# Kernel tuning notes

Hardware: AMD Instinct MI355X
Metric: run time of the kernel (lower is better)

## Reference

```python
import jax, jax.numpy as jnp
import numpy as np
import math

N_HEADS = 16
ROPE_BASE = 10000.0


def _rope_interleaved(t, cos, sin):
    # t: [B,H,T,dk]; cos/sin: [T, dk//2] broadcast over B,H
    te, to = t[..., 0::2], t[..., 1::2]
    re = te * cos - to * sin
    ro = te * sin + to * cos
    # interleave back: [..., dk//2, 2] -> [..., dk]
    return jnp.stack([re, ro], axis=-1).reshape(t.shape)


def setup_inputs() -> dict:
    key = jax.random.key(0)
    ks = jax.random.split(key, 5)
    B, T, C = 2, 2048, 1024
    s = 1.0 / math.sqrt(C)
    return {
        "x": jax.random.normal(ks[0], (B, T, C), dtype=jnp.float32),
        "W_qkv": jax.random.normal(ks[1], (C, 3 * C), dtype=jnp.float32) * s,
        "b_qkv": jax.random.normal(ks[2], (3 * C,), dtype=jnp.float32) * 0.02,
        "W_proj": jax.random.normal(ks[3], (C, C), dtype=jnp.float32) * s,
        "b_proj": jax.random.normal(ks[4], (C,), dtype=jnp.float32) * 0.02,
    }


def reference(x, W_qkv, b_qkv, W_proj, b_proj):
    B, T, C = x.shape
    H = N_HEADS
    dk = C // H

    qkv = x @ W_qkv + b_qkv                      # [B,T,3C]
    q, k, v = jnp.split(qkv, 3, axis=-1)
    q = q.reshape(B, T, H, dk).transpose(0, 2, 1, 3)  # [B,H,T,dk]
    k = k.reshape(B, T, H, dk).transpose(0, 2, 1, 3)
    v = v.reshape(B, T, H, dk).transpose(0, 2, 1, 3)

    # RoPE angles: pos * base^(-2i/dk)
    freqs = ROPE_BASE ** (-2.0 * jnp.arange(dk // 2, dtype=jnp.float32) / dk)
    angles = jnp.arange(T, dtype=jnp.float32)[:, None] * freqs[None, :]  # [T,dk//2]
    cos, sin = jnp.cos(angles), jnp.sin(angles)

    q = _rope_interleaved(q, cos, sin)
    k = _rope_interleaved(k, cos, sin)

    attn = jnp.einsum("bhqd,bhkd->bhqk", q, k) / math.sqrt(dk)  # [B,H,T,T]
    causal = jnp.triu(jnp.full((T, T), -jnp.inf, dtype=attn.dtype), k=1)
    attn = jax.nn.softmax(attn + causal, axis=-1)

    scores = jnp.einsum("bhqk,bhkd->bhqd", attn, v)  # [B,H,T,dk]
    scores = scores.transpose(0, 2, 1, 3).reshape(B, T, C)
    return scores @ W_proj + b_proj
```

## Files before the change

### kernel.cpp

```cpp
#include <hip/hip_runtime.h>
#include <hip/hip_bf16.h>

typedef __bf16 bf16x8 __attribute__((ext_vector_type(8)));
typedef float f32x4 __attribute__((ext_vector_type(4)));
typedef float f32x16 __attribute__((ext_vector_type(16)));
typedef unsigned short u16;
typedef u16 u16x8 __attribute__((ext_vector_type(8)));

__device__ __forceinline__ u16 f2bf(float f) {
  union { float f; unsigned u; } v; v.f = f;
  unsigned r = v.u + 0x7fffu + ((v.u >> 16) & 1u);
  return (u16)(r >> 16);
}
__device__ __forceinline__ float bf2f(u16 u) {
  union { unsigned u; float f; } v; v.u = (unsigned)u << 16; return v.f;
}
__device__ __forceinline__ unsigned cvtpk(float a, float b) {
  unsigned r;
  asm("v_cvt_pk_bf16_f32 %0, %1, %2" : "=v"(r) : "v"(a), "v"(b));
  return r;
}
__device__ __forceinline__ float exp2_(float x) {
  float r;
  asm("v_exp_f32 %0, %1" : "=v"(r) : "v"(x));
  return r;
}
__device__ __forceinline__ void gload16(const void* g, void* l) {
  __builtin_amdgcn_global_load_lds(
      (__attribute__((address_space(1))) void*)(void*)g,
      (__attribute__((address_space(3))) void*)l, 16, 0, 0);
}

union U8 { bf16x8 v; unsigned u[4]; };

__global__ __launch_bounds__(256) void cast_x_k(const float* __restrict__ x,
                                                u16* __restrict__ xb, int n8) {
  int id = blockIdx.x * 256 + threadIdx.x;
  if (id >= n8) return;
  const float4* p = (const float4*)(x + (size_t)id * 8);
  float4 a = p[0], b = p[1];
  u16x8 o;
  o[0] = f2bf(a.x); o[1] = f2bf(a.y); o[2] = f2bf(a.z); o[3] = f2bf(a.w);
  o[4] = f2bf(b.x); o[5] = f2bf(b.y); o[6] = f2bf(b.z); o[7] = f2bf(b.w);
  *(u16x8*)(xb + (size_t)id * 8) = o;
}

__global__ __launch_bounds__(256) void tcast_k(const float* __restrict__ W,
                                               u16* __restrict__ Wt, int R, int Cc) {
  __shared__ float tile[32][33];
  int bx = blockIdx.x * 32, by = blockIdx.y * 32;
  int tx = threadIdx.x & 31, ty = threadIdx.x >> 5;
#pragma unroll
  for (int j = 0; j < 4; j++)
    tile[ty + j * 8][tx] = W[(size_t)(by + ty + j * 8) * Cc + bx + tx];
  __syncthreads();
#pragma unroll
  for (int j = 0; j < 4; j++)
    Wt[(size_t)(bx + ty + j * 8) * R + by + tx] = f2bf(tile[tx][ty + j * 8]);
}

template <bool BF16OUT>
__global__ __launch_bounds__(256) void gemm_bt_k(const u16* __restrict__ A,
                                                 const u16* __restrict__ Bt,
                                                 const float* __restrict__ bias,
                                                 void* __restrict__ Cv,
                                                 int M, int N, int K) {
  __shared__ u16 As[128 * 64];
  __shared__ u16 Bs[128 * 64];
  int tid = threadIdx.x;
  int m0 = blockIdx.y * 128, n0 = blockIdx.x * 128;
  int wave = tid >> 6, lane = tid & 63;
  int wm = (wave & 1) * 64, wn = (wave >> 1) * 64;
  int lrow = lane & 15, lk = (lane >> 4) * 8;
  int rr = lane >> 3, cb = (lane & 7) * 16;

  f32x4 acc[4][4] = {};

  for (int k0 = 0; k0 < K; k0 += 64) {
#pragma unroll
    for (int i = 0; i < 4; i++) {
      int row = wave * 32 + i * 8 + rr;
      int cc = (cb ^ ((row & 7) << 4)) >> 1;
      gload16(A + (size_t)(m0 + row) * K + k0 + cc, &As[(wave * 32 + i * 8) * 64]);
      gload16(Bt + (size_t)(n0 + row) * K + k0 + cc, &Bs[(wave * 32 + i * 8) * 64]);
    }
    __syncthreads();
#pragma unroll
    for (int kk = 0; kk < 2; kk++) {
      bf16x8 af[4], bfr[4];
#pragma unroll
      for (int i = 0; i < 4; i++) {
        int arow = wm + i * 16 + lrow;
        int ab = (arow * 128 + (kk * 32 + lk) * 2) ^ ((arow & 7) << 4);
        af[i] = *(const bf16x8*)((const char*)As + ab);
        int brow = wn + i * 16 + lrow;
        int bb = (brow * 128 + (kk * 32 + lk) * 2) ^ ((brow & 7) << 4);
        bfr[i] = *(const bf16x8*)((const char*)Bs + bb);
      }
#pragma unroll
      for (int i = 0; i < 4; i++)
#pragma unroll
        for (int j = 0; j < 4; j++)
          acc[i][j] = __builtin_amdgcn_mfma_f32_16x16x32_bf16(af[i], bfr[j], acc[i][j], 0, 0, 0);
    }
    __syncthreads();
  }
  int rg = lane >> 4;
#pragma unroll
  for (int i = 0; i < 4; i++) {
#pragma unroll
    for (int j = 0; j < 4; j++) {
      int col = n0 + wn + j * 16 + lrow;
      float bz = bias ? bias[col] : 0.f;
#pragma unroll
      for (int r = 0; r < 4; r++) {
        int row = m0 + wm + i * 16 + rg * 4 + r;
        float val = acc[i][j][r] + bz;
        if constexpr (BF16OUT)
          ((u16*)Cv)[(size_t)row * N + col] = f2bf(val);
        else
          ((float*)Cv)[(size_t)row * N + col] = val;
      }
    }
  }
}

__global__ __launch_bounds__(256) void rope_qk_k(const u16* __restrict__ qkv,
                                                 u16* __restrict__ qb,
                                                 u16* __restrict__ kfb) {
  int id = blockIdx.x * 256 + threadIdx.x;
  int i = id & 31;
  int h = (id >> 5) & 15;
  int t = (id >> 9) & 2047;
  int b = id >> 20;
  size_t row = (size_t)b * 2048 + t;
  const u16* base = qkv + row * 3072 + h * 64 + 2 * i;
  ushort2 qp = *(const ushort2*)(base);
  ushort2 kp = *(const ushort2*)(base + 1024);
  float qx = bf2f(qp.x), qy = bf2f(qp.y), kx = bf2f(kp.x), ky = bf2f(kp.y);
  float freq = exp2f((float)i * -0.41524101186092029f);
  float ang = (float)t * freq;
  float sv, cv;
  sincosf(ang, &sv, &cv);
  const float QS = 0.18033688011112042f;
  int bh = b * 16 + h;
  size_t obase = (((size_t)bh * 2048) + t) * 64 + 2 * i;
  ushort2 qo, ko;
  qo.x = f2bf((qx * cv - qy * sv) * QS); qo.y = f2bf((qx * sv + qy * cv) * QS);
  ko.x = f2bf(kx * cv - ky * sv);        ko.y = f2bf(kx * sv + ky * cv);
  *(ushort2*)(qb + obase) = qo;
  int de = 2 * i;
  size_t kidx = (((size_t)bh * 32 + (t >> 6)) * 2 + ((t >> 5) & 1)) * 2048 +
                (de >> 4) * 512 + (((de >> 3) & 1) * 32 + (t & 31)) * 8 + (de & 7);
  *(ushort2*)(kfb + kidx) = ko;
}

__global__ __launch_bounds__(256) void v_pack_k(const u16* __restrict__ qkv,
                                                u16* __restrict__ vf) {
  __shared__ u16 tl[64][72];
  int bh = blockIdx.x, kt = blockIdx.y;
  int b = bh >> 4, h = bh & 15;
  int tid = threadIdx.x;
#pragma unroll
  for (int rep = 0; rep < 2; rep++) {
    int tr = rep * 32 + (tid >> 3);
    int dc = (tid & 7) * 8;
    u16x8 v = *(const u16x8*)(qkv + ((size_t)(b * 2048 + kt * 64 + tr)) * 3072 + 2048 + h * 64 + dc);
    *(u16x8*)&tl[tr][dc] = v;
  }
  __syncthreads();
  u16* dst = vf + ((size_t)bh * 32 + kt) * 4096;
#pragma unroll
  for (int rep = 0; rep < 2; rep++) {
    int c = rep * 256 + tid;
    int dh = c >> 8, s = (c >> 6) & 3, l = c & 63;
    int hi = l >> 5, ql = l & 31;
    u16x8 o;
#pragma unroll
    for (int j = 0; j < 8; j++) o[j] = tl[s * 16 + hi * 8 + j][dh * 32 + ql];
    *(u16x8*)(dst + (size_t)c * 8) = o;
  }
}


#define ATT_PREF(Pa, Pb, IT)                                                      \
  do {                                                                            \
    const u16* kb_ = KfP + (size_t)(IT) * 4096 + ln8;                             \
    _Pragma("unroll") for (int d_ = 0; d_ < 4; d_++) {                            \
      Pa[d_] = *(const bf16x8*)(kb_ + d_ * 512);                                  \
      Pb[d_] = *(const bf16x8*)(kb_ + 2048 + d_ * 512);                           \
    }                                                                             \
  } while (0)

#define ATT_BODY(Pa, Pb, IT)                                                      \
  do {                                                                            \
    int kv0_ = (IT) * 64;                                                         \
    const u16* vb_ = VfP + (size_t)(IT) * 4096 + ln8;                             \
    f32x16 sa = {}, sb = {};                                                      \
    _Pragma("unroll") for (int d_ = 0; d_ < 4; d_++) {                            \
      sa = __builtin_amdgcn_mfma_f32_32x32x16_bf16(Pa[d_], qf[d_], sa, 0, 0, 0);  \
      sb = __builtin_amdgcn_mfma_f32_32x32x16_bf16(Pb[d_], qf[d_], sb, 0, 0, 0);  \
    }                                                                             \
    bf16x8 v0_[4], v1_[4];                                                        \
    _Pragma("unroll") for (int s_ = 0; s_ < 4; s_++) {                            \
      v0_[s_] = *(const bf16x8*)(vb_ + s_ * 512);                                 \
      v1_[s_] = *(const bf16x8*)(vb_ + 2048 + s_ * 512);                          \
    }                                                                             \
    if ((IT) == nIter - 1) {                                                      \
      _Pragma("unroll") for (int r_ = 0; r_ < 16; r_++) {                         \
        int ro_ = (r_ & 3) + 8 * (r_ >> 2) + 4 * hi;                              \
        if (kv0_ + ro_ > qg) sa[r_] = -3e38f;                                     \
        if (kv0_ + 32 + ro_ > qg) sb[r_] = -3e38f;                                \
      }                                                                           \
    }                                                                             \
    float ta_ = -3e38f, tb_ = -3e38f;                                             \
    _Pragma("unroll") for (int r_ = 0; r_ < 8; r_++) {                            \
      ta_ = fmaxf(ta_, fmaxf(sa[r_], sa[r_ + 8]));                                \
      tb_ = fmaxf(tb_, fmaxf(sb[r_], sb[r_ + 8]));                                \
    }                                                                             \
    float tmax_ = fmaxf(ta_, tb_);                                                \
    tmax_ = fmaxf(tmax_, __shfl_xor(tmax_, 32));                                  \
    if (!__all(tmax_ <= m + 11.5409f)) {                                          \
      float mn_ = fmaxf(m, tmax_);                                                \
      float corr_ = exp2_(m - mn_);                                               \
      m = mn_;                                                                    \
      ls[0] *= corr_;                                                             \
      _Pragma("unroll") for (int r_ = 0; r_ < 16; r_++) {                         \
        o0[r_] *= corr_; o1[r_] *= corr_;                                         \
      }                                                                           \
    }                                                                             \
    _Pragma("unroll") for (int r_ = 0; r_ < 16; r_++) {                           \
      sa[r_] = exp2_(sa[r_] - m);                                                 \
      sb[r_] = exp2_(sb[r_] - m);                                                 \
    }                                                                             \
    unsigned wA_[8], xA_[8], wB_[8], xB_[8];                                      \
    _Pragma("unroll") for (int j_ = 0; j_ < 8; j_++) {                            \
      wA_[j_] = cvtpk(sa[2 * j_], sa[2 * j_ + 1]);                                \
      wB_[j_] = cvtpk(sb[2 * j_], sb[2 * j_ + 1]);                                \
    }                                                                             \
    _Pragma("unroll") for (int j_ = 0; j_ < 8; j_++) {                            \
      xA_[j_] = (unsigned)__shfl_xor((int)wA_[j_], 32);                           \
      xB_[j_] = (unsigned)__shfl_xor((int)wB_[j_], 32);                           \
    }                                                                             \
    U8 pf0_, pf1_, pf2_, pf3_;                                                    \
    pf0_.u[0] = hi ? xA_[2] : wA_[0]; pf0_.u[1] = hi ? xA_[3] : wA_[1];           \
    pf0_.u[2] = hi ? wA_[2] : xA_[0]; pf0_.u[3] = hi ? wA_[3] : xA_[1];           \
    pf1_.u[0] = hi ? xA_[6] : wA_[4]; pf1_.u[1] = hi ? xA_[7] : wA_[5];           \
    pf1_.u[2] = hi ? wA_[6] : xA_[4]; pf1_.u[3] = hi ? wA_[7] : xA_[5];           \
    pf2_.u[0] = hi ? xB_[2] : wB_[0]; pf2_.u[1] = hi ? xB_[3] : wB_[1];           \
    pf2_.u[2] = hi ? wB_[2] : xB_[0]; pf2_.u[3] = hi ? wB_[3] : xB_[1];           \
    pf3_.u[0] = hi ? xB_[6] : wB_[4]; pf3_.u[1] = hi ? xB_[7] : wB_[5];           \
    pf3_.u[2] = hi ? wB_[6] : xB_[4]; pf3_.u[3] = hi ? wB_[7] : xB_[5];           \
    o0 = __builtin_amdgcn_mfma_f32_32x32x16_bf16(v0_[0], pf0_.v, o0, 0, 0, 0);    \
    o1 = __builtin_amdgcn_mfma_f32_32x32x16_bf16(v1_[0], pf0_.v, o1, 0, 0, 0);    \
    o0 = __builtin_amdgcn_mfma_f32_32x32x16_bf16(v0_[1], pf1_.v, o0, 0, 0, 0);    \
    o1 = __builtin_amdgcn_mfma_f32_32x32x16_bf16(v1_[1], pf1_.v, o1, 0, 0, 0);    \
    o0 = __builtin_amdgcn_mfma_f32_32x32x16_bf16(v0_[2], pf2_.v, o0, 0, 0, 0);    \
    o1 = __builtin_amdgcn_mfma_f32_32x32x16_bf16(v1_[2], pf2_.v, o1, 0, 0, 0);    \
    o0 = __builtin_amdgcn_mfma_f32_32x32x16_bf16(v0_[3], pf3_.v, o0, 0, 0, 0);    \
    o1 = __builtin_amdgcn_mfma_f32_32x32x16_bf16(v1_[3], pf3_.v, o1, 0, 0, 0);    \
    ls = __builtin_amdgcn_mfma_f32_32x32x16_bf16(onesf.v, pf0_.v, ls, 0, 0, 0);   \
    ls = __builtin_amdgcn_mfma_f32_32x32x16_bf16(onesf.v, pf1_.v, ls, 0, 0, 0);   \
    ls = __builtin_amdgcn_mfma_f32_32x32x16_bf16(onesf.v, pf2_.v, ls, 0, 0, 0);   \
    ls = __builtin_amdgcn_mfma_f32_32x32x16_bf16(onesf.v, pf3_.v, ls, 0, 0, 0);   \
  } while (0)

__global__ __launch_bounds__(64) void attn_k(const u16* __restrict__ Q,
                                             const u16* __restrict__ Kf,
                                             const u16* __restrict__ Vf,
                                             u16* __restrict__ Os) {
  const int T = 2048;
  int blk = blockIdx.x;
  int g = blk & 7;
  int bh = g * 4 + ((blk >> 3) & 3);
  int p = blk >> 5;
  int lane = threadIdx.x & 63;
  int ql = lane & 31, hi = lane >> 5, hq = hi * 8;
  int ln8 = lane * 8;
  const u16* Qp = Q + (size_t)bh * T * 64;
  const u16* KfP = Kf + (size_t)bh * 32 * 4096;
  const u16* VfP = Vf + (size_t)bh * 32 * 4096;
  int b = bh >> 4, h = bh & 15;

  U8 onesf;
#pragma unroll
  for (int j = 0; j < 4; j++) onesf.u[j] = 0x3F803F80u;

#pragma unroll 1
  for (int ph = 0; ph < 2; ph++) {
    const int qt = ph ? 63 - p : p;
    const int qw0 = qt * 32;
    const int qg = qw0 + ql;
    const int nIter = (qt >> 1) + 1;

    bf16x8 qf[4];
#pragma unroll
    for (int ds = 0; ds < 4; ds++)
      qf[ds] = *(const bf16x8*)(Qp + (size_t)(qw0 + ql) * 64 + ds * 16 + hq);

    f32x16 o0 = {}, o1 = {}, ls = {};
    float m = -1e30f;

    bf16x8 Aa[4], Ab[4], Ba[4], Bb[4];
    ATT_PREF(Aa, Ab, 0);
    int it = 0;
    while (true) {
      if (it + 1 < nIter) ATT_PREF(Ba, Bb, it + 1);
      ATT_BODY(Aa, Ab, it);
      if (++it >= nIter) break;
      if (it + 1 < nIter) ATT_PREF(Aa, Ab, it + 1);
      ATT_BODY(Ba, Bb, it);
      if (++it >= nIter) break;
    }

    float inv = 1.f / ls[0];
    u16* orow = Os + ((size_t)(b * T + qg)) * 1024 + h * 64;
#pragma unroll
    for (int j = 0; j < 4; j++) {
      ushort4 o;
      o.x = f2bf(o0[4 * j + 0] * inv); o.y = f2bf(o0[4 * j + 1] * inv);
      o.z = f2bf(o0[4 * j + 2] * inv); o.w = f2bf(o0[4 * j + 3] * inv);
      *(ushort4*)(orow + 8 * j + 4 * hi) = o;
      ushort4 q;
      q.x = f2bf(o1[4 * j + 0] * inv); q.y = f2bf(o1[4 * j + 1] * inv);
      q.z = f2bf(o1[4 * j + 2] * inv); q.w = f2bf(o1[4 * j + 3] * inv);
      *(ushort4*)(orow + 32 + 8 * j + 4 * hi) = q;
    }
  }
}

extern "C" void kernel_launch(void* const* d_in, const int* in_sizes, int n_in,
                              void* d_out, int out_size, void* d_ws, size_t ws_size,
                              hipStream_t stream) {
  const float* x      = (const float*)d_in[0];
  const float* W_qkv  = (const float*)d_in[1];
  const float* b_qkv  = (const float*)d_in[2];
  const float* W_proj = (const float*)d_in[3];
  const float* b_proj = (const float*)d_in[4];
  float* out = (float*)d_out;

  const int B = 2, T = 2048, C = 1024;
  const int M = B * T;

  char* ws = (char*)d_ws;
  u16* xb     = (u16*)(ws);
  u16* wqkvt  = (u16*)(ws + (8ull << 20));
  u16* wprojt = (u16*)(ws + (14ull << 20));
  u16* qb     = (u16*)(ws + (16ull << 20));
  u16* kfb    = (u16*)(ws + (24ull << 20));
  u16* vfb    = (u16*)(ws + (32ull << 20));
  u16* sc     = (u16*)(ws + (40ull << 20));
  u16* qkvb   = (u16*)(ws + (48ull << 20));

  cast_x_k<<<(M * C / 8 + 255) / 256, 256, 0, stream>>>(x, xb, M * C / 8);
  tcast_k<<<dim3(3 * C / 32, C / 32), 256, 0, stream>>>(W_qkv, wqkvt, C, 3 * C);
  tcast_k<<<dim3(C / 32, C / 32), 256, 0, stream>>>(W_proj, wprojt, C, C);
  gemm_bt_k<true><<<dim3(3 * C / 128, M / 128), 256, 0, stream>>>(xb, wqkvt, b_qkv, qkvb, M, 3 * C, C);
  rope_qk_k<<<(B * T * 16 * 32) / 256, 256, 0, stream>>>(qkvb, qb, kfb);
  v_pack_k<<<dim3(B * 16, T / 64), 256, 0, stream>>>(qkvb, vfb);
  attn_k<<<1024, 64, 0, stream>>>(qb, kfb, vfb, sc);
  gemm_bt_k<false><<<dim3(C / 128, M / 128), 256, 0, stream>>>(sc, wprojt, b_proj, out, M, C, C);
}
```

Before: 132.9 us.

## Split attention KV loop across two waves with shared-memory softmax merge

The attention kernel now launches two waves per block. Each wave processes alternate KV tiles for the same 32-query tile, and the two partial results (o, max, sum) are combined through shared memory using a flash-decoding-style rescale before the output is written. Q is also written by the RoPE kernel in an MFMA-fragment layout, so each lane loads its Q fragment contiguously. This doubles the number of resident waves to hide latency, at the cost of shared-memory traffic, two barriers per phase, and uneven tile counts between the waves.

```diff
diff --git a/kernel.cpp b/kernel.cpp
--- a/kernel.cpp
+++ b/kernel.cpp
@@ -126,7 +126,7 @@
 }
 
 __global__ __launch_bounds__(256) void rope_qk_k(const u16* __restrict__ qkv,
-                                                 u16* __restrict__ qb,
+                                                 u16* __restrict__ qfb,
                                                  u16* __restrict__ kfb) {
   int id = blockIdx.x * 256 + threadIdx.x;
   int i = id & 31;
@@ -144,14 +144,15 @@
   sincosf(ang, &sv, &cv);
   const float QS = 0.18033688011112042f;
   int bh = b * 16 + h;
-  size_t obase = (((size_t)bh * 2048) + t) * 64 + 2 * i;
   ushort2 qo, ko;
   qo.x = f2bf((qx * cv - qy * sv) * QS); qo.y = f2bf((qx * sv + qy * cv) * QS);
   ko.x = f2bf(kx * cv - ky * sv);        ko.y = f2bf(kx * sv + ky * cv);
-  *(ushort2*)(qb + obase) = qo;
   int de = 2 * i;
+  int ds = de >> 4, hb = (de >> 3) & 1, j = de & 7;
+  size_t qidx = ((size_t)bh * 64 + (t >> 5)) * 2048 + ds * 512 + (hb * 32 + (t & 31)) * 8 + j;
+  *(ushort2*)(qfb + qidx) = qo;
   size_t kidx = (((size_t)bh * 32 + (t >> 6)) * 2 + ((t >> 5) & 1)) * 2048 +
-                (de >> 4) * 512 + (((de >> 3) & 1) * 32 + (t & 31)) * 8 + (de & 7);
+                ds * 512 + (hb * 32 + (t & 31)) * 8 + j;
   *(ushort2*)(kfb + kidx) = ko;
 }
 
@@ -265,19 +266,22 @@
     ls = __builtin_amdgcn_mfma_f32_32x32x16_bf16(onesf.v, pf3_.v, ls, 0, 0, 0);   \
   } while (0)
 
-__global__ __launch_bounds__(64) void attn_k(const u16* __restrict__ Q,
-                                             const u16* __restrict__ Kf,
-                                             const u16* __restrict__ Vf,
-                                             u16* __restrict__ Os) {
+__global__ __launch_bounds__(128) void attn_k(const u16* __restrict__ Qf,
+                                              const u16* __restrict__ Kf,
+                                              const u16* __restrict__ Vf,
+                                              u16* __restrict__ Os) {
+  __shared__ float smO[64][33];
+  __shared__ float smM[64], smL[64];
   const int T = 2048;
   int blk = blockIdx.x;
   int g = blk & 7;
   int bh = g * 4 + ((blk >> 3) & 3);
   int p = blk >> 5;
+  int wave = threadIdx.x >> 6;
   int lane = threadIdx.x & 63;
-  int ql = lane & 31, hi = lane >> 5, hq = hi * 8;
+  int ql = lane & 31, hi = lane >> 5;
   int ln8 = lane * 8;
-  const u16* Qp = Q + (size_t)bh * T * 64;
+  const u16* QfP = Qf + (size_t)bh * 64 * 2048;
   const u16* KfP = Kf + (size_t)bh * 32 * 4096;
   const u16* VfP = Vf + (size_t)bh * 32 * 4096;
   int b = bh >> 4, h = bh & 15;
@@ -289,43 +293,69 @@
 #pragma unroll 1
   for (int ph = 0; ph < 2; ph++) {
     const int qt = ph ? 63 - p : p;
-    const int qw0 = qt * 32;
-    const int qg = qw0 + ql;
+    const int qg = qt * 32 + ql;
     const int nIter = (qt >> 1) + 1;
+    const int par = wave ^ ph;
 
     bf16x8 qf[4];
 #pragma unroll
     for (int ds = 0; ds < 4; ds++)
-      qf[ds] = *(const bf16x8*)(Qp + (size_t)(qw0 + ql) * 64 + ds * 16 + hq);
+      qf[ds] = *(const bf16x8*)(QfP + (size_t)qt * 2048 + ds * 512 + ln8);
 
     f32x16 o0 = {}, o1 = {}, ls = {};
     float m = -1e30f;
 
     bf16x8 Aa[4], Ab[4], Ba[4], Bb[4];
-    ATT_PREF(Aa, Ab, 0);
-    int it = 0;
-    while (true) {
-      if (it + 1 < nIter) ATT_PREF(Ba, Bb, it + 1);
-      ATT_BODY(Aa, Ab, it);
-      if (++it >= nIter) break;
-      if (it + 1 < nIter) ATT_PREF(Aa, Ab, it + 1);
-      ATT_BODY(Ba, Bb, it);
-      if (++it >= nIter) break;
-    }
-
-    float inv = 1.f / ls[0];
-    u16* orow = Os + ((size_t)(b * T + qg)) * 1024 + h * 64;
-#pragma unroll
-    for (int j = 0; j < 4; j++) {
-      ushort4 o;
-      o.x = f2bf(o0[4 * j + 0] * inv); o.y = f2bf(o0[4 * j + 1] * inv);
-      o.z = f2bf(o0[4 * j + 2] * inv); o.w = f2bf(o0[4 * j + 3] * inv);
-      *(ushort4*)(orow + 8 * j + 4 * hi) = o;
-      ushort4 q;
-      q.x = f2bf(o1[4 * j + 0] * inv); q.y = f2bf(o1[4 * j + 1] * inv);
-      q.z = f2bf(o1[4 * j + 2] * inv); q.w = f2bf(o1[4 * j + 3] * inv);
-      *(ushort4*)(orow + 32 + 8 * j + 4 * hi) = q;
-    }
+    int it = par;
+    if (it < nIter) {
+      ATT_PREF(Aa, Ab, it);
+      while (true) {
+        if (it + 2 < nIter) ATT_PREF(Ba, Bb, it + 2);
+        ATT_BODY(Aa, Ab, it);
+        it += 2;
+        if (it >= nIter) break;
+        if (it + 2 < nIter) ATT_PREF(Aa, Ab, it + 2);
+        ATT_BODY(Ba, Bb, it);
+        it += 2;
+        if (it >= nIter) break;
+      }
+    }
+
+    if (wave == 1) {
+#pragma unroll
+      for (int r = 0; r < 16; r++) {
+        smO[lane][r] = o0[r];
+        smO[lane][16 + r] = o1[r];
+      }
+      smM[lane] = m;
+      smL[lane] = ls[0];
+    }
+    __syncthreads();
+    if (wave == 0) {
+      float m1 = smM[lane], l1 = smL[lane];
+      float mt = fmaxf(m, m1);
+      float a0 = exp2_(m - mt), a1 = exp2_(m1 - mt);
+      float lt = ls[0] * a0 + l1 * a1;
+      float inv = 1.f / lt;
+      float c0 = a0 * inv, c1 = a1 * inv;
+      u16* orow = Os + ((size_t)(b * T + qg)) * 1024 + h * 64;
+#pragma unroll
+      for (int j = 0; j < 4; j++) {
+        ushort4 o;
+        o.x = f2bf(o0[4 * j + 0] * c0 + smO[lane][4 * j + 0] * c1);
+        o.y = f2bf(o0[4 * j + 1] * c0 + smO[lane][4 * j + 1] * c1);
+        o.z = f2bf(o0[4 * j + 2] * c0 + smO[lane][4 * j + 2] * c1);
+        o.w = f2bf(o0[4 * j + 3] * c0 + smO[lane][4 * j + 3] * c1);
+        *(ushort4*)(orow + 8 * j + 4 * hi) = o;
+        ushort4 q2;
+        q2.x = f2bf(o1[4 * j + 0] * c0 + smO[lane][16 + 4 * j + 0] * c1);
+        q2.y = f2bf(o1[4 * j + 1] * c0 + smO[lane][16 + 4 * j + 1] * c1);
+        q2.z = f2bf(o1[4 * j + 2] * c0 + smO[lane][16 + 4 * j + 2] * c1);
+        q2.w = f2bf(o1[4 * j + 3] * c0 + smO[lane][16 + 4 * j + 3] * c1);
+        *(ushort4*)(orow + 32 + 8 * j + 4 * hi) = q2;
+      }
+    }
+    __syncthreads();
   }
 }
 
@@ -346,7 +376,7 @@
   u16* xb     = (u16*)(ws);
   u16* wqkvt  = (u16*)(ws + (8ull << 20));
   u16* wprojt = (u16*)(ws + (14ull << 20));
-  u16* qb     = (u16*)(ws + (16ull << 20));
+  u16* qfb    = (u16*)(ws + (16ull << 20));
   u16* kfb    = (u16*)(ws + (24ull << 20));
   u16* vfb    = (u16*)(ws + (32ull << 20));
   u16* sc     = (u16*)(ws + (40ull << 20));
@@ -356,8 +386,8 @@
   tcast_k<<<dim3(3 * C / 32, C / 32), 256, 0, stream>>>(W_qkv, wqkvt, C, 3 * C);
   tcast_k<<<dim3(C / 32, C / 32), 256, 0, stream>>>(W_proj, wprojt, C, C);
   gemm_bt_k<true><<<dim3(3 * C / 128, M / 128), 256, 0, stream>>>(xb, wqkvt, b_qkv, qkvb, M, 3 * C, C);
-  rope_qk_k<<<(B * T * 16 * 32) / 256, 256, 0, stream>>>(qkvb, qb, kfb);
+  rope_qk_k<<<(B * T * 16 * 32) / 256, 256, 0, stream>>>(qkvb, qfb, kfb);
   v_pack_k<<<dim3(B * 16, T / 64), 256, 0, stream>>>(qkvb, vfb);
-  attn_k<<<1024, 64, 0, stream>>>(qb, kfb, vfb, sc);
+  attn_k<<<1024, 128, 0, stream>>>(qfb, kfb, vfb, sc);
   gemm_bt_k<false><<<dim3(C / 128, M / 128), 256, 0, stream>>>(sc, wprojt, b_proj, out, M, C, C);
 }
```

Measured after the change: 146.1 us. 1.1x slower.

## Software-pipeline QK MFMA with softmax, one q-tile per block, permlane swaps

Applied to the files above, without the earlier changes.

The attention kernel now computes the next tile's QK^T scores while the current tile goes through softmax and PV, with K prefetched two tiles ahead. Each block now owns a single 32-row query tile (2048 blocks, launched longest-first) instead of pairing tiles p and 63-p. Q is written by the RoPE kernel in a fragment-packed layout so it loads as contiguous vectors. The cross-half shuffles plus selects are replaced with v_permlane32_swap. These aim to hide MFMA and exp latency, simplify Q loads and cut shuffle overhead, at the cost of more registers and more blocks to schedule.

```diff
diff --git a/kernel.cpp b/kernel.cpp
--- a/kernel.cpp
+++ b/kernel.cpp
@@ -126,7 +126,7 @@
 }
 
 __global__ __launch_bounds__(256) void rope_qk_k(const u16* __restrict__ qkv,
-                                                 u16* __restrict__ qb,
+                                                 u16* __restrict__ qfb,
                                                  u16* __restrict__ kfb) {
   int id = blockIdx.x * 256 + threadIdx.x;
   int i = id & 31;
@@ -144,14 +144,15 @@
   sincosf(ang, &sv, &cv);
   const float QS = 0.18033688011112042f;
   int bh = b * 16 + h;
-  size_t obase = (((size_t)bh * 2048) + t) * 64 + 2 * i;
   ushort2 qo, ko;
   qo.x = f2bf((qx * cv - qy * sv) * QS); qo.y = f2bf((qx * sv + qy * cv) * QS);
   ko.x = f2bf(kx * cv - ky * sv);        ko.y = f2bf(kx * sv + ky * cv);
-  *(ushort2*)(qb + obase) = qo;
   int de = 2 * i;
+  int ds = de >> 4, hb = (de >> 3) & 1, j = de & 7;
+  size_t qidx = ((size_t)bh * 64 + (t >> 5)) * 2048 + ds * 512 + (hb * 32 + (t & 31)) * 8 + j;
+  *(ushort2*)(qfb + qidx) = qo;
   size_t kidx = (((size_t)bh * 32 + (t >> 6)) * 2 + ((t >> 5) & 1)) * 2048 +
-                (de >> 4) * 512 + (((de >> 3) & 1) * 32 + (t & 31)) * 8 + (de & 7);
+                ds * 512 + (hb * 32 + (t & 31)) * 8 + j;
   *(ushort2*)(kfb + kidx) = ko;
 }
 
@@ -183,40 +184,48 @@
 }
 
 
-#define ATT_PREF(Pa, Pb, IT)                                                      \
+#define KPREF(K0, K1, IT)                                                         \
   do {                                                                            \
     const u16* kb_ = KfP + (size_t)(IT) * 4096 + ln8;                             \
     _Pragma("unroll") for (int d_ = 0; d_ < 4; d_++) {                            \
-      Pa[d_] = *(const bf16x8*)(kb_ + d_ * 512);                                  \
-      Pb[d_] = *(const bf16x8*)(kb_ + 2048 + d_ * 512);                           \
+      K0[d_] = *(const bf16x8*)(kb_ + d_ * 512);                                  \
+      K1[d_] = *(const bf16x8*)(kb_ + 2048 + d_ * 512);                           \
     }                                                                             \
   } while (0)
 
-#define ATT_BODY(Pa, Pb, IT)                                                      \
+#define QKC(SA, SB, K0, K1)                                                       \
   do {                                                                            \
-    int kv0_ = (IT) * 64;                                                         \
+    SA = (f32x16){};                                                              \
+    SB = (f32x16){};                                                              \
+    _Pragma("unroll") for (int d_ = 0; d_ < 4; d_++) {                            \
+      SA = __builtin_amdgcn_mfma_f32_32x32x16_bf16(K0[d_], qf[d_], SA, 0, 0, 0);  \
+      SB = __builtin_amdgcn_mfma_f32_32x32x16_bf16(K1[d_], qf[d_], SB, 0, 0, 0);  \
+    }                                                                             \
+  } while (0)
+
+#define VLOADM(IT)                                                                \
+  do {                                                                            \
     const u16* vb_ = VfP + (size_t)(IT) * 4096 + ln8;                             \
-    f32x16 sa = {}, sb = {};                                                      \
-    _Pragma("unroll") for (int d_ = 0; d_ < 4; d_++) {                            \
-      sa = __builtin_amdgcn_mfma_f32_32x32x16_bf16(Pa[d_], qf[d_], sa, 0, 0, 0);  \
-      sb = __builtin_amdgcn_mfma_f32_32x32x16_bf16(Pb[d_], qf[d_], sb, 0, 0, 0);  \
-    }                                                                             \
-    bf16x8 v0_[4], v1_[4];                                                        \
     _Pragma("unroll") for (int s_ = 0; s_ < 4; s_++) {                            \
-      v0_[s_] = *(const bf16x8*)(vb_ + s_ * 512);                                 \
-      v1_[s_] = *(const bf16x8*)(vb_ + 2048 + s_ * 512);                          \
-    }                                                                             \
-    if ((IT) == nIter - 1) {                                                      \
+      vv0[s_] = *(const bf16x8*)(vb_ + s_ * 512);                                 \
+      vv1[s_] = *(const bf16x8*)(vb_ + 2048 + s_ * 512);                          \
+    }                                                                             \
+  } while (0)
+
+#define SMPV(SA, SB, IT, LASTF)                                                   \
+  do {                                                                            \
+    if (LASTF) {                                                                  \
+      int kv0_ = (IT) * 64;                                                       \
       _Pragma("unroll") for (int r_ = 0; r_ < 16; r_++) {                         \
         int ro_ = (r_ & 3) + 8 * (r_ >> 2) + 4 * hi;                              \
-        if (kv0_ + ro_ > qg) sa[r_] = -3e38f;                                     \
-        if (kv0_ + 32 + ro_ > qg) sb[r_] = -3e38f;                                \
+        if (kv0_ + ro_ > qg) SA[r_] = -3e38f;                                     \
+        if (kv0_ + 32 + ro_ > qg) SB[r_] = -3e38f;                                \
       }                                                                           \
     }                                                                             \
     float ta_ = -3e38f, tb_ = -3e38f;                                             \
     _Pragma("unroll") for (int r_ = 0; r_ < 8; r_++) {                            \
-      ta_ = fmaxf(ta_, fmaxf(sa[r_], sa[r_ + 8]));                                \
-      tb_ = fmaxf(tb_, fmaxf(sb[r_], sb[r_ + 8]));                                \
+      ta_ = fmaxf(ta_, fmaxf(SA[r_], SA[r_ + 8]));                                \
+      tb_ = fmaxf(tb_, fmaxf(SB[r_], SB[r_ + 8]));                                \
     }                                                                             \
     float tmax_ = fmaxf(ta_, tb_);                                                \
     tmax_ = fmaxf(tmax_, __shfl_xor(tmax_, 32));                                  \
@@ -230,42 +239,45 @@
       }                                                                           \
     }                                                                             \
     _Pragma("unroll") for (int r_ = 0; r_ < 16; r_++) {                           \
-      sa[r_] = exp2_(sa[r_] - m);                                                 \
-      sb[r_] = exp2_(sb[r_] - m);                                                 \
-    }                                                                             \
-    unsigned wA_[8], xA_[8], wB_[8], xB_[8];                                      \
-    _Pragma("unroll") for (int j_ = 0; j_ < 8; j_++) {                            \
-      wA_[j_] = cvtpk(sa[2 * j_], sa[2 * j_ + 1]);                                \
-      wB_[j_] = cvtpk(sb[2 * j_], sb[2 * j_ + 1]);                                \
-    }                                                                             \
-    _Pragma("unroll") for (int j_ = 0; j_ < 8; j_++) {                            \
-      xA_[j_] = (unsigned)__shfl_xor((int)wA_[j_], 32);                           \
-      xB_[j_] = (unsigned)__shfl_xor((int)wB_[j_], 32);                           \
-    }                                                                             \
+      SA[r_] = exp2_(SA[r_] - m);                                                 \
+      SB[r_] = exp2_(SB[r_] - m);                                                 \
+    }                                                                             \
+    unsigned w0_ = cvtpk(SA[0], SA[1]),   w1_ = cvtpk(SA[2], SA[3]);              \
+    unsigned w2_ = cvtpk(SA[4], SA[5]),   w3_ = cvtpk(SA[6], SA[7]);              \
+    unsigned w4_ = cvtpk(SA[8], SA[9]),   w5_ = cvtpk(SA[10], SA[11]);            \
+    unsigned w6_ = cvtpk(SA[12], SA[13]), w7_ = cvtpk(SA[14], SA[15]);            \
+    unsigned y0_ = cvtpk(SB[0], SB[1]),   y1_ = cvtpk(SB[2], SB[3]);              \
+    unsigned y2_ = cvtpk(SB[4], SB[5]),   y3_ = cvtpk(SB[6], SB[7]);              \
+    unsigned y4_ = cvtpk(SB[8], SB[9]),   y5_ = cvtpk(SB[10], SB[11]);            \
+    unsigned y6_ = cvtpk(SB[12], SB[13]), y7_ = cvtpk(SB[14], SB[15]);            \
+    asm("v_permlane32_swap_b32 %0, %1" : "+v"(w0_), "+v"(w2_));                   \
+    asm("v_permlane32_swap_b32 %0, %1" : "+v"(w1_), "+v"(w3_));                   \
+    asm("v_permlane32_swap_b32 %0, %1" : "+v"(w4_), "+v"(w6_));                   \
+    asm("v_permlane32_swap_b32 %0, %1" : "+v"(w5_), "+v"(w7_));                   \
+    asm("v_permlane32_swap_b32 %0, %1" : "+v"(y0_), "+v"(y2_));                   \
+    asm("v_permlane32_swap_b32 %0, %1" : "+v"(y1_), "+v"(y3_));                   \
+    asm("v_permlane32_swap_b32 %0, %1" : "+v"(y4_), "+v"(y6_));                   \
+    asm("v_permlane32_swap_b32 %0, %1" : "+v"(y5_), "+v"(y7_));                   \
     U8 pf0_, pf1_, pf2_, pf3_;                                                    \
-    pf0_.u[0] = hi ? xA_[2] : wA_[0]; pf0_.u[1] = hi ? xA_[3] : wA_[1];           \
-    pf0_.u[2] = hi ? wA_[2] : xA_[0]; pf0_.u[3] = hi ? wA_[3] : xA_[1];           \
-    pf1_.u[0] = hi ? xA_[6] : wA_[4]; pf1_.u[1] = hi ? xA_[7] : wA_[5];           \
-    pf1_.u[2] = hi ? wA_[6] : xA_[4]; pf1_.u[3] = hi ? wA_[7] : xA_[5];           \
-    pf2_.u[0] = hi ? xB_[2] : wB_[0]; pf2_.u[1] = hi ? xB_[3] : wB_[1];           \
-    pf2_.u[2] = hi ? wB_[2] : xB_[0]; pf2_.u[3] = hi ? wB_[3] : xB_[1];           \
-    pf3_.u[0] = hi ? xB_[6] : wB_[4]; pf3_.u[1] = hi ? xB_[7] : wB_[5];           \
-    pf3_.u[2] = hi ? wB_[6] : xB_[4]; pf3_.u[3] = hi ? wB_[7] : xB_[5];           \
-    o0 = __builtin_amdgcn_mfma_f32_32x32x16_bf16(v0_[0], pf0_.v, o0, 0, 0, 0);    \
-    o1 = __builtin_amdgcn_mfma_f32_32x32x16_bf16(v1_[0], pf0_.v, o1, 0, 0, 0);    \
-    o0 = __builtin_amdgcn_mfma_f32_32x32x16_bf16(v0_[1], pf1_.v, o0, 0, 0, 0);    \
-    o1 = __builtin_amdgcn_mfma_f32_32x32x16_bf16(v1_[1], pf1_.v, o1, 0, 0, 0);    \
-    o0 = __builtin_amdgcn_mfma_f32_32x32x16_bf16(v0_[2], pf2_.v, o0, 0, 0, 0);    \
-    o1 = __builtin_amdgcn_mfma_f32_32x32x16_bf16(v1_[2], pf2_.v, o1, 0, 0, 0);    \
-    o0 = __builtin_amdgcn_mfma_f32_32x32x16_bf16(v0_[3], pf3_.v, o0, 0, 0, 0);    \
-    o1 = __builtin_amdgcn_mfma_f32_32x32x16_bf16(v1_[3], pf3_.v, o1, 0, 0, 0);    \
+    pf0_.u[0] = w0_; pf0_.u[1] = w1_; pf0_.u[2] = w2_; pf0_.u[3] = w3_;           \
+    pf1_.u[0] = w4_; pf1_.u[1] = w5_; pf1_.u[2] = w6_; pf1_.u[3] = w7_;           \
+    pf2_.u[0] = y0_; pf2_.u[1] = y1_; pf2_.u[2] = y2_; pf2_.u[3] = y3_;           \
+    pf3_.u[0] = y4_; pf3_.u[1] = y5_; pf3_.u[2] = y6_; pf3_.u[3] = y7_;           \
+    o0 = __builtin_amdgcn_mfma_f32_32x32x16_bf16(vv0[0], pf0_.v, o0, 0, 0, 0);    \
+    o1 = __builtin_amdgcn_mfma_f32_32x32x16_bf16(vv1[0], pf0_.v, o1, 0, 0, 0);    \
+    o0 = __builtin_amdgcn_mfma_f32_32x32x16_bf16(vv0[1], pf1_.v, o0, 0, 0, 0);    \
+    o1 = __builtin_amdgcn_mfma_f32_32x32x16_bf16(vv1[1], pf1_.v, o1, 0, 0, 0);    \
+    o0 = __builtin_amdgcn_mfma_f32_32x32x16_bf16(vv0[2], pf2_.v, o0, 0, 0, 0);    \
+    o1 = __builtin_amdgcn_mfma_f32_32x32x16_bf16(vv1[2], pf2_.v, o1, 0, 0, 0);    \
+    o0 = __builtin_amdgcn_mfma_f32_32x32x16_bf16(vv0[3], pf3_.v, o0, 0, 0, 0);    \
+    o1 = __builtin_amdgcn_mfma_f32_32x32x16_bf16(vv1[3], pf3_.v, o1, 0, 0, 0);    \
     ls = __builtin_amdgcn_mfma_f32_32x32x16_bf16(onesf.v, pf0_.v, ls, 0, 0, 0);   \
     ls = __builtin_amdgcn_mfma_f32_32x32x16_bf16(onesf.v, pf1_.v, ls, 0, 0, 0);   \
     ls = __builtin_amdgcn_mfma_f32_32x32x16_bf16(onesf.v, pf2_.v, ls, 0, 0, 0);   \
     ls = __builtin_amdgcn_mfma_f32_32x32x16_bf16(onesf.v, pf3_.v, ls, 0, 0, 0);   \
   } while (0)
 
-__global__ __launch_bounds__(64) void attn_k(const u16* __restrict__ Q,
+__global__ __launch_bounds__(64) void attn_k(const u16* __restrict__ Qf,
                                              const u16* __restrict__ Kf,
                                              const u16* __restrict__ Vf,
                                              u16* __restrict__ Os) {
@@ -273,11 +285,13 @@
   int blk = blockIdx.x;
   int g = blk & 7;
   int bh = g * 4 + ((blk >> 3) & 3);
-  int p = blk >> 5;
+  int qt = 63 - (blk >> 5);
   int lane = threadIdx.x & 63;
-  int ql = lane & 31, hi = lane >> 5, hq = hi * 8;
+  int ql = lane & 31, hi = lane >> 5;
   int ln8 = lane * 8;
-  const u16* Qp = Q + (size_t)bh * T * 64;
+  int qg = qt * 32 + ql;
+  int nIter = (qt >> 1) + 1;
+  const u16* QfP = Qf + (size_t)bh * 64 * 2048;
   const u16* KfP = Kf + (size_t)bh * 32 * 4096;
   const u16* VfP = Vf + (size_t)bh * 32 * 4096;
   int b = bh >> 4, h = bh & 15;
@@ -286,46 +300,51 @@
 #pragma unroll
   for (int j = 0; j < 4; j++) onesf.u[j] = 0x3F803F80u;
 
-#pragma unroll 1
-  for (int ph = 0; ph < 2; ph++) {
-    const int qt = ph ? 63 - p : p;
-    const int qw0 = qt * 32;
-    const int qg = qw0 + ql;
-    const int nIter = (qt >> 1) + 1;
-
-    bf16x8 qf[4];
-#pragma unroll
-    for (int ds = 0; ds < 4; ds++)
-      qf[ds] = *(const bf16x8*)(Qp + (size_t)(qw0 + ql) * 64 + ds * 16 + hq);
-
-    f32x16 o0 = {}, o1 = {}, ls = {};
-    float m = -1e30f;
-
-    bf16x8 Aa[4], Ab[4], Ba[4], Bb[4];
-    ATT_PREF(Aa, Ab, 0);
-    int it = 0;
-    while (true) {
-      if (it + 1 < nIter) ATT_PREF(Ba, Bb, it + 1);
-      ATT_BODY(Aa, Ab, it);
-      if (++it >= nIter) break;
-      if (it + 1 < nIter) ATT_PREF(Aa, Ab, it + 1);
-      ATT_BODY(Ba, Bb, it);
-      if (++it >= nIter) break;
-    }
-
-    float inv = 1.f / ls[0];
-    u16* orow = Os + ((size_t)(b * T + qg)) * 1024 + h * 64;
-#pragma unroll
-    for (int j = 0; j < 4; j++) {
-      ushort4 o;
-      o.x = f2bf(o0[4 * j + 0] * inv); o.y = f2bf(o0[4 * j + 1] * inv);
-      o.z = f2bf(o0[4 * j + 2] * inv); o.w = f2bf(o0[4 * j + 3] * inv);
-      *(ushort4*)(orow + 8 * j + 4 * hi) = o;
-      ushort4 q;
-      q.x = f2bf(o1[4 * j + 0] * inv); q.y = f2bf(o1[4 * j + 1] * inv);
-      q.z = f2bf(o1[4 * j + 2] * inv); q.w = f2bf(o1[4 * j + 3] * inv);
-      *(ushort4*)(orow + 32 + 8 * j + 4 * hi) = q;
-    }
+  bf16x8 qf[4];
+#pragma unroll
+  for (int ds = 0; ds < 4; ds++)
+    qf[ds] = *(const bf16x8*)(QfP + (size_t)qt * 2048 + ds * 512 + ln8);
+
+  f32x16 o0 = {}, o1 = {}, ls = {};
+  float m = -1e30f;
+
+  bf16x8 Ka0[4], Ka1[4], Kb0[4], Kb1[4], vv0[4], vv1[4];
+  f32x16 sA0, sA1, sB0, sB1;
+
+  KPREF(Ka0, Ka1, 0);
+  QKC(sA0, sA1, Ka0, Ka1);
+  if (nIter > 1) KPREF(Kb0, Kb1, 1);
+
+  int t = 0;
+  for (;;) {
+    bool last = (t == nIter - 1);
+    VLOADM(t);
+    if (t + 2 < nIter) KPREF(Ka0, Ka1, t + 2);
+    if (!last) QKC(sB0, sB1, Kb0, Kb1);
+    SMPV(sA0, sA1, t, last);
+    if (last) break;
+    ++t;
+    last = (t == nIter - 1);
+    VLOADM(t);
+    if (t + 2 < nIter) KPREF(Kb0, Kb1, t + 2);
+    if (!last) QKC(sA0, sA1, Ka0, Ka1);
+    SMPV(sB0, sB1, t, last);
+    if (last) break;
+    ++t;
+  }
+
+  float inv = 1.f / ls[0];
+  u16* orow = Os + ((size_t)(b * T + qg)) * 1024 + h * 64;
+#pragma unroll
+  for (int j = 0; j < 4; j++) {
+    ushort4 o;
+    o.x = f2bf(o0[4 * j + 0] * inv); o.y = f2bf(o0[4 * j + 1] * inv);
+    o.z = f2bf(o0[4 * j + 2] * inv); o.w = f2bf(o0[4 * j + 3] * inv);
+    *(ushort4*)(orow + 8 * j + 4 * hi) = o;
+    ushort4 q2;
+    q2.x = f2bf(o1[4 * j + 0] * inv); q2.y = f2bf(o1[4 * j + 1] * inv);
+    q2.z = f2bf(o1[4 * j + 2] * inv); q2.w = f2bf(o1[4 * j + 3] * inv);
+    *(ushort4*)(orow + 32 + 8 * j + 4 * hi) = q2;
   }
 }
 
@@ -346,7 +365,7 @@
   u16* xb     = (u16*)(ws);
   u16* wqkvt  = (u16*)(ws + (8ull << 20));
   u16* wprojt = (u16*)(ws + (14ull << 20));
-  u16* qb     = (u16*)(ws + (16ull << 20));
+  u16* qfb    = (u16*)(ws + (16ull << 20));
   u16* kfb    = (u16*)(ws + (24ull << 20));
   u16* vfb    = (u16*)(ws + (32ull << 20));
   u16* sc     = (u16*)(ws + (40ull << 20));
@@ -356,8 +375,8 @@
   tcast_k<<<dim3(3 * C / 32, C / 32), 256, 0, stream>>>(W_qkv, wqkvt, C, 3 * C);
   tcast_k<<<dim3(C / 32, C / 32), 256, 0, stream>>>(W_proj, wprojt, C, C);
   gemm_bt_k<true><<<dim3(3 * C / 128, M / 128), 256, 0, stream>>>(xb, wqkvt, b_qkv, qkvb, M, 3 * C, C);
-  rope_qk_k<<<(B * T * 16 * 32) / 256, 256, 0, stream>>>(qkvb, qb, kfb);
+  rope_qk_k<<<(B * T * 16 * 32) / 256, 256, 0, stream>>>(qkvb, qfb, kfb);
   v_pack_k<<<dim3(B * 16, T / 64), 256, 0, stream>>>(qkvb, vfb);
-  attn_k<<<1024, 64, 0, stream>>>(qb, kfb, vfb, sc);
+  attn_k<<<2048, 64, 0, stream>>>(qfb, kfb, vfb, sc);
   gemm_bt_k<false><<<dim3(C / 128, M / 128), 256, 0, stream>>>(sc, wprojt, b_proj, out, M, C, C);
 }
```

Result: slower. 139.0 us (+4.6%).
